# Kernel optimization log

Hardware: AMD Instinct MI355X
Metric: run time of the kernel (lower is better)

The kernel has to match this reference:

```python
import jax, jax.numpy as jnp
import numpy as np

B, AUDIO, FRAME = 4, 327680, 80
HID, NH, NKV, HD, FFN, NL = 320, 8, 4, 40, 1280, 6
WINDOWS = ((16, 4), (16, 4), (16, 0), (16, 0), (16, 4), (16, 4))


def _ln(x, w, eps=1e-5):
    m = x.mean(-1, keepdims=True)
    c = x - m
    v = (c * c).mean(-1, keepdims=True)
    return c * jax.lax.rsqrt(v + eps) * w


def _causal_conv(x, w, b, stride, left_pad):
    # x: [B, C_in, T]; w: [C_out, C_in, K] (torch Conv1d layout); causal left pad
    x = jnp.pad(x, ((0, 0), (0, 0), (left_pad, 0)))
    y = jax.lax.conv_general_dilated(x, w, (stride,), [(0, 0)],
                                     dimension_numbers=('NCH', 'OIH', 'NCH'))
    return y + b[None, :, None]


def _mask_conv(mask, stride, left_pad, ksize):
    # propagate bool validity mask through a strided causal conv
    mf = jnp.pad(mask.astype(jnp.float32)[:, None, :], ((0, 0), (0, 0), (left_pad, 0)))
    w1 = jnp.ones((1, 1, ksize), jnp.float32)
    mc = jax.lax.conv_general_dilated(mf, w1, (stride,), [(0, 0)],
                                      dimension_numbers=('NCH', 'OIH', 'NCH'))
    return mc[:, 0] > 0


def _window_mask(T, lw, rw, dtype):
    # additive mask: 0 where 0<=q-k<lw or 0<k-q<rw, else -inf; [1,1,T,T]
    d = jnp.arange(T)[:, None] - jnp.arange(T)[None, :]
    ok = ((d >= 0) & (d < lw)) | ((d < 0) & (-d < rw))
    return jnp.where(ok, jnp.zeros((), dtype), jnp.full((), -jnp.inf, dtype))[None, None]


def _encode(input_values, padding_mask, log_k, lin_w, conv1_w, conv1_b,
            conv2_w, conv2_b, ln1_w, q_w, k_w, v_w, o_w, ln2_w,
            fc1_w, fc2_w, final_ln_w):
    Bn = input_values.shape[0]
    x = input_values.reshape(Bn, -1, FRAME)               # [B, Tf, 80]
    # per-frame CMVN
    c = x - x.mean(-1, keepdims=True)
    x = c / jnp.sqrt((c * c).mean(-1, keepdims=True) + 1e-6)
    # learnable asinh compression
    x = jnp.arcsinh(jnp.exp(log_k) * x)
    x = jax.nn.silu(x @ lin_w.T)                          # [B, Tf, HID]
    Tf = x.shape[1]
    num_frames = padding_mask.sum(-1) // FRAME
    fmask = jnp.arange(Tf)[None, :] < num_frames[:, None]  # [B, Tf]
    x = x * fmask[..., None].astype(x.dtype)
    x = x.transpose(0, 2, 1)                              # [B, HID, Tf]
    # conv1: 320 -> 640, k=5, s=2, causal
    x = _causal_conv(x, conv1_w, conv1_b, 2, 4)
    m1 = _mask_conv(fmask, 2, 4, 5)
    x = jax.nn.silu(x * m1[:, None].astype(x.dtype))
    # conv2: 640 -> 320, k=5, s=2, causal
    m2 = _mask_conv(m1, 2, 4, 5)
    x = _causal_conv(x, conv2_w, conv2_b, 2, 4) * m2[:, None].astype(x.dtype)
    x = x.transpose(0, 2, 1)                              # [B, Tenc, HID]
    Tenc = x.shape[1]
    kpm = jnp.where(m2, jnp.zeros((), x.dtype), jnp.full((), -jnp.inf, x.dtype))[:, None, None, :]
    n_rep = NH // NKV
    scale = 1.0 / np.sqrt(HD).astype(np.float32)
    for i in range(NL):
        lw, rw = WINDOWS[i]
        wm = _window_mask(Tenc, lw, rw, x.dtype)
        h = _ln(x, ln1_w[i])
        q = (h @ q_w[i].T).reshape(Bn, Tenc, NH, HD).transpose(0, 2, 1, 3)
        k = (h @ k_w[i].T).reshape(Bn, Tenc, NKV, HD).transpose(0, 2, 1, 3)
        v = (h @ v_w[i].T).reshape(Bn, Tenc, NKV, HD).transpose(0, 2, 1, 3)
        k = jnp.repeat(k, n_rep, axis=1)                  # GQA repeat_kv
        v = jnp.repeat(v, n_rep, axis=1)
        s = jnp.einsum('bhqd,bhkd->bhqk', q, k) * scale + wm + kpm
        a = jax.nn.softmax(s, axis=-1)
        o = jnp.einsum('bhqk,bhkd->bhqd', a, v).transpose(0, 2, 1, 3).reshape(Bn, Tenc, HID)
        x = x + o @ o_w[i].T
        h = _ln(x, ln2_w[i])
        x = x + jax.nn.silu(h @ fc1_w[i].T) @ fc2_w[i].T
    return _ln(x, final_ln_w)


def setup_inputs() -> dict:
    key = jax.random.key(0)
    ks = iter(jax.random.split(key, 20))
    def w(shape, fan_in):
        return jax.random.normal(next(ks), shape, jnp.float32) / np.sqrt(fan_in).astype(np.float32)
    return {
        'input_values': jax.random.normal(next(ks), (B, AUDIO), jnp.float32),
        'padding_mask': jnp.ones((B, AUDIO), bool),
        'log_k': jnp.log(jnp.float32(0.75)),
        'lin_w': w((HID, FRAME), FRAME),
        'conv1_w': w((2 * HID, HID, 5), HID * 5), 'conv1_b': jnp.zeros((2 * HID,), jnp.float32),
        'conv2_w': w((HID, 2 * HID, 5), 2 * HID * 5), 'conv2_b': jnp.zeros((HID,), jnp.float32),
        'ln1_w': jnp.ones((NL, HID), jnp.float32),
        'q_w': w((NL, NH * HD, HID), HID),
        'k_w': w((NL, NKV * HD, HID), HID),
        'v_w': w((NL, NKV * HD, HID), HID),
        'o_w': w((NL, HID, NH * HD), NH * HD),
        'ln2_w': jnp.ones((NL, HID), jnp.float32),
        'fc1_w': w((NL, FFN, HID), HID),
        'fc2_w': w((NL, HID, FFN), FFN),
        'final_ln_w': jnp.ones((HID,), jnp.float32),
    }


def reference(input_values, padding_mask, log_k, lin_w, conv1_w, conv1_b,
              conv2_w, conv2_b, ln1_w, q_w, k_w, v_w, o_w, ln2_w,
              fc1_w, fc2_w, final_ln_w):
    return _encode(input_values, padding_mask, log_k, lin_w, conv1_w, conv1_b,
                   conv2_w, conv2_b, ln1_w, q_w, k_w, v_w, o_w, ln2_w,
                   fc1_w, fc2_w, final_ln_w)
```

## Files before the change

### kernel.cpp

```cpp
#include <hip/hip_runtime.h>
#include <hip/hip_bf16.h>
#include <math.h>


typedef __attribute__((ext_vector_type(8))) short short8;
typedef __attribute__((ext_vector_type(4))) float floatx4;

__device__ __forceinline__ float silu_f(float x) {
    return x / (1.0f + expf(-x));
}

__device__ __forceinline__ unsigned short f2bf(float x) {
    union { float f; unsigned int u; } v; v.f = x;
    unsigned int r = v.u + 0x7fffu + ((v.u >> 16) & 1u);
    return (unsigned short)(r >> 16);
}

__global__ void cvt_bf16(const float* __restrict__ s, unsigned short* __restrict__ d, int n) {
    int i = blockIdx.x * 256 + threadIdx.x;
    if (i < n) d[i] = f2bf(s[i]);
}

__global__ void pack_qkv(const float* __restrict__ qw, const float* __restrict__ kw,
                         const float* __restrict__ vw, unsigned short* __restrict__ d) {
    int i = blockIdx.x * 256 + threadIdx.x;
    if (i >= 6 * 640 * 320) return;
    int l = i / (640 * 320);
    int r = i - l * (640 * 320);
    int n = r / 320, c = r - (r / 320) * 320;
    float val;
    if (n < 320)      val = qw[((size_t)l * 320 + n) * 320 + c];
    else if (n < 480) val = kw[((size_t)l * 160 + (n - 320)) * 320 + c];
    else              val = vw[((size_t)l * 160 + (n - 480)) * 320 + c];
    d[i] = f2bf(val);
}

__global__ void prep_conv_w(const float* __restrict__ w, unsigned short* __restrict__ wt,
                            int Cout, int Cin) {
    int i = blockIdx.x * 256 + threadIdx.x;
    int total = Cout * Cin * 5;
    if (i >= total) return;
    int o = i / (Cin * 5);
    int rem = i - o * (Cin * 5);
    int c = rem / 5, k = rem - c * 5;
    wt[(size_t)o * (5 * Cin) + k * Cin + c] = f2bf(w[i]);
}

__global__ void prep_lin(const float* __restrict__ w, unsigned short* __restrict__ wt) {
    int i = blockIdx.x * 256 + threadIdx.x;
    if (i >= 320 * 128) return;
    int o = i >> 7, c = i & 127;
    wt[i] = (c < 80) ? f2bf(w[o * 80 + c]) : (unsigned short)0;
}

__global__ void cmvn_asinh_kernel(const float* __restrict__ in, const float* __restrict__ logk,
                                  unsigned short* __restrict__ zb) {
    __shared__ float raw[640];
    __shared__ float mS[8], iS[8];
    int f0 = blockIdx.x * 8;
    int tid = threadIdx.x;

    for (int e = tid; e < 640; e += 320)
        raw[e] = in[(size_t)f0 * 80 + e];
    __syncthreads();

    if (tid < 8) {
        float s = 0.f, ss = 0.f;
        for (int j = 0; j < 80; ++j) {
            float v = raw[tid * 80 + j];
            s += v; ss += v * v;
        }
        float m = s * (1.0f / 80.0f);
        float var = ss * (1.0f / 80.0f) - m * m;
        mS[tid] = m;
        iS[tid] = rsqrtf(var + 1e-6f);
    }
    __syncthreads();

    float ek = expf(logk[0]);
    for (int e = tid; e < 1024; e += 320) {
        int f = e >> 7, c = e & 127;
        unsigned short v = 0;
        if (c < 80) {
            float t = ek * (raw[f * 80 + c] - mS[f]) * iS[f];
            v = f2bf(asinhf(t));
        }
        zb[(size_t)(f0 + f) * 128 + c] = v;
    }
}

__global__ void im2col1(const unsigned short* __restrict__ x0, unsigned short* __restrict__ A1) {
    int idx = blockIdx.x * 256 + threadIdx.x;
    if (idx >= 8192 * 5 * 40) return;
    int c8 = idx % 40;
    int tmp = idx / 40;
    int kk = tmp % 5;
    int row = tmp / 5;
    int b = row >> 11, t = row & 2047;
    int sr = 2 * t + kk - 4;
    uint4 val = make_uint4(0u, 0u, 0u, 0u);
    if (sr >= 0) val = *(const uint4*)&x0[((size_t)b * 4096 + sr) * 320 + c8 * 8];
    *(uint4*)&A1[(size_t)row * 1600 + kk * 320 + c8 * 8] = val;
}

__global__ void im2col2(const unsigned short* __restrict__ y1, unsigned short* __restrict__ A2) {
    int idx = blockIdx.x * 256 + threadIdx.x;
    if (idx >= 4096 * 5 * 80) return;
    int c8 = idx % 80;
    int tmp = idx / 80;
    int kk = tmp % 5;
    int row = tmp / 5;
    int b = row >> 10, t = row & 1023;
    int sr = 2 * t + kk - 4;
    uint4 val = make_uint4(0u, 0u, 0u, 0u);
    if (sr >= 0) val = *(const uint4*)&y1[((size_t)b * 2048 + sr) * 640 + c8 * 8];
    *(uint4*)&A2[(size_t)row * 3200 + kk * 640 + c8 * 8] = val;
}

__global__ __launch_bounds__(256) void mfma_gemm(
    const unsigned short* __restrict__ A, const unsigned short* __restrict__ W,
    int M, int N, int K, int ldc,
    float* __restrict__ Cf, unsigned short* __restrict__ Cb,
    const float* __restrict__ bias, const float* __restrict__ res, int act_silu) {
    __shared__ unsigned short As[64 * 64];
    __shared__ unsigned short Bs[64 * 64];
    int m0 = blockIdx.x * 64;
    int n0 = blockIdx.y * 64;
    int tid = threadIdx.x;
    int wave = tid >> 6, lane = tid & 63;
    int lm = lane & 15, lq = lane >> 4;
    int wm = (wave & 1) * 32, wn = (wave >> 1) * 32;

    int lr = lane >> 3;
    int lg = (lane & 7) ^ lr;
    int rw0 = wave * 16;
    const unsigned short* a0 = A + (size_t)(m0 + rw0 + lr) * K + lg * 8;
    const unsigned short* a1 = A + (size_t)(m0 + rw0 + 8 + lr) * K + lg * 8;
    const unsigned short* b0 = W + (size_t)(n0 + rw0 + lr) * K + lg * 8;
    const unsigned short* b1 = W + (size_t)(n0 + rw0 + 8 + lr) * K + lg * 8;
    unsigned short* la0 = &As[rw0 * 64];
    unsigned short* la1 = &As[(rw0 + 8) * 64];
    unsigned short* lb0 = &Bs[rw0 * 64];
    unsigned short* lb1 = &Bs[(rw0 + 8) * 64];

    floatx4 acc[2][2];
#pragma unroll
    for (int i = 0; i < 2; ++i)
#pragma unroll
        for (int j = 0; j < 2; ++j) acc[i][j] = (floatx4)0.0f;

    int swl = lm & 7;

    for (int k0 = 0; k0 < K; k0 += 64) {
        __builtin_amdgcn_global_load_lds((const __attribute__((address_space(1))) void*)(a0 + k0),
                                         (__attribute__((address_space(3))) void*)la0, 16, 0, 0);
        __builtin_amdgcn_global_load_lds((const __attribute__((address_space(1))) void*)(a1 + k0),
                                         (__attribute__((address_space(3))) void*)la1, 16, 0, 0);
        __builtin_amdgcn_global_load_lds((const __attribute__((address_space(1))) void*)(b0 + k0),
                                         (__attribute__((address_space(3))) void*)lb0, 16, 0, 0);
        __builtin_amdgcn_global_load_lds((const __attribute__((address_space(1))) void*)(b1 + k0),
                                         (__attribute__((address_space(3))) void*)lb1, 16, 0, 0);
        __syncthreads();
#pragma unroll
        for (int ks = 0; ks < 2; ++ks) {
            int gg = ks * 4 + lq;
            short8 a[2], b[2];
#pragma unroll
            for (int i = 0; i < 2; ++i) {
                int r = wm + i * 16 + lm;
                a[i] = *(const short8*)&As[r * 64 + ((gg ^ swl)) * 8];
            }
#pragma unroll
            for (int j = 0; j < 2; ++j) {
                int r = wn + j * 16 + lm;
                b[j] = *(const short8*)&Bs[r * 64 + ((gg ^ swl)) * 8];
            }
#pragma unroll
            for (int i = 0; i < 2; ++i)
#pragma unroll
                for (int j = 0; j < 2; ++j)
                    acc[i][j] = __builtin_amdgcn_mfma_f32_16x16x32_bf16(a[i], b[j], acc[i][j], 0, 0, 0);
        }
        __syncthreads();
    }

#pragma unroll
    for (int j = 0; j < 2; ++j) {
        int n = n0 + wn + j * 16 + lm;
        float bv = bias ? bias[n] : 0.0f;
#pragma unroll
        for (int i = 0; i < 2; ++i) {
#pragma unroll
            for (int r = 0; r < 4; ++r) {
                int m = m0 + wm + i * 16 + lq * 4 + r;
                float v = acc[i][j][r] + bv;
                if (act_silu) v = silu_f(v);
                if (res) v += res[(size_t)m * ldc + n];
                if (Cf) Cf[(size_t)m * ldc + n] = v;
                else Cb[(size_t)m * ldc + n] = f2bf(v);
            }
        }
    }
}

__global__ __launch_bounds__(256) void ln_kernel(
    const float* __restrict__ x, const float* __restrict__ w,
    float* __restrict__ yf, unsigned short* __restrict__ yb) {
    int row = blockIdx.x * 4 + (threadIdx.x >> 6);
    int lane = threadIdx.x & 63;
    const float* xr = x + (size_t)row * 320;
    float v[5];
    float s = 0.f, ss = 0.f;
#pragma unroll
    for (int i = 0; i < 5; ++i) {
        v[i] = xr[lane + i * 64];
        s += v[i]; ss += v[i] * v[i];
    }
#pragma unroll
    for (int o = 32; o > 0; o >>= 1) {
        s += __shfl_down(s, o);
        ss += __shfl_down(ss, o);
    }
    s = __shfl(s, 0);
    ss = __shfl(ss, 0);
    float m = s * (1.0f / 320.0f);
    float rstd = rsqrtf(ss * (1.0f / 320.0f) - m * m + 1e-5f);
#pragma unroll
    for (int i = 0; i < 5; ++i) {
        float o_ = (v[i] - m) * rstd * w[lane + i * 64];
        if (yf) yf[(size_t)row * 320 + lane + i * 64] = o_;
        else yb[(size_t)row * 320 + lane + i * 64] = f2bf(o_);
    }
}

#define AROWS 82
#define APAD 44
__global__ __launch_bounds__(128) void attn_kernel(
    const float* __restrict__ qkv, unsigned short* __restrict__ o, int T, int rw) {
    __shared__ float Ks[AROWS * APAD];
    __shared__ float Vs[AROWS * APAD];
    int t0 = blockIdx.x * 64;
    int g = blockIdx.y, b = blockIdx.z;
    int tid = threadIdx.x;
    const float scale = 0.1581138830084190f;

    const float* base_k = qkv + (size_t)b * T * 640 + 320 + g * 40;
    const float* base_v = qkv + (size_t)b * T * 640 + 480 + g * 40;
    int rbase = t0 - 15;
    for (int idx = tid; idx < AROWS * 10; idx += 128) {
        int row = idx / 10, d4 = idx - row * 10;
        int gr = min(max(rbase + row, 0), T - 1);
        *(float4*)&Ks[row * APAD + d4 * 4] = *(const float4*)&base_k[(size_t)gr * 640 + d4 * 4];
        *(float4*)&Vs[row * APAD + d4 * 4] = *(const float4*)&base_v[(size_t)gr * 640 + d4 * 4];
    }
    __syncthreads();

    int q = tid >> 1;
    int hh = tid & 1;
    int t = t0 + q;
    int h = g * 2 + hh;

    const float* qrow = qkv + ((size_t)(b * T + t)) * 640 + h * 40;
    float qv[40];
#pragma unroll
    for (int d4 = 0; d4 < 10; ++d4) {
        float4 v4 = *(const float4*)&qrow[d4 * 4];
        qv[d4 * 4 + 0] = v4.x; qv[d4 * 4 + 1] = v4.y;
        qv[d4 * 4 + 2] = v4.z; qv[d4 * 4 + 3] = v4.w;
    }

    int kmaxoff = (rw > 0) ? (rw - 1) : 0;
    float s[19];
#pragma unroll
    for (int j = 0; j < 19; ++j) {
        int kk = t - 15 + j;
        const float* kr = &Ks[(q + j) * APAD];
        float acc = 0.f;
#pragma unroll
        for (int d4 = 0; d4 < 10; ++d4) {
            float4 k4 = *(const float4*)&kr[d4 * 4];
            acc = fmaf(qv[d4 * 4 + 0], k4.x, acc);
            acc = fmaf(qv[d4 * 4 + 1], k4.y, acc);
            acc = fmaf(qv[d4 * 4 + 2], k4.z, acc);
            acc = fmaf(qv[d4 * 4 + 3], k4.w, acc);
        }
        bool valid = (kk >= 0) && (kk < T) && (kk <= t + kmaxoff);
        s[j] = valid ? acc * scale : -1e30f;
    }

    float mx = -1e30f;
#pragma unroll
    for (int j = 0; j < 19; ++j) mx = fmaxf(mx, s[j]);
    float l = 0.f;
#pragma unroll
    for (int j = 0; j < 19; ++j) {
        s[j] = expf(s[j] - mx);
        l += s[j];
    }
    float inv = 1.0f / l;

    float ov[40];
#pragma unroll
    for (int d = 0; d < 40; ++d) ov[d] = 0.f;
#pragma unroll
    for (int j = 0; j < 19; ++j) {
        const float* vr = &Vs[(q + j) * APAD];
        float p = s[j] * inv;
#pragma unroll
        for (int d4 = 0; d4 < 10; ++d4) {
            float4 v4 = *(const float4*)&vr[d4 * 4];
            ov[d4 * 4 + 0] = fmaf(p, v4.x, ov[d4 * 4 + 0]);
            ov[d4 * 4 + 1] = fmaf(p, v4.y, ov[d4 * 4 + 1]);
            ov[d4 * 4 + 2] = fmaf(p, v4.z, ov[d4 * 4 + 2]);
            ov[d4 * 4 + 3] = fmaf(p, v4.w, ov[d4 * 4 + 3]);
        }
    }

    unsigned short* orow = o + ((size_t)(b * T + t)) * 320 + h * 40;
#pragma unroll
    for (int d2 = 0; d2 < 20; ++d2) {
        unsigned int lo = f2bf(ov[d2 * 2]);
        unsigned int hi = f2bf(ov[d2 * 2 + 1]);
        *(unsigned int*)&orow[d2 * 2] = lo | (hi << 16);
    }
}

extern "C" void kernel_launch(void* const* d_in, const int* in_sizes, int n_in,
                              void* d_out, int out_size, void* d_ws, size_t ws_size,
                              hipStream_t stream) {
    const float* input_values = (const float*)d_in[0];
    const float* log_k   = (const float*)d_in[2];
    const float* lin_w   = (const float*)d_in[3];
    const float* conv1_w = (const float*)d_in[4];
    const float* conv1_b = (const float*)d_in[5];
    const float* conv2_w = (const float*)d_in[6];
    const float* conv2_b = (const float*)d_in[7];
    const float* ln1_w   = (const float*)d_in[8];
    const float* q_w     = (const float*)d_in[9];
    const float* k_w     = (const float*)d_in[10];
    const float* v_w     = (const float*)d_in[11];
    const float* o_w     = (const float*)d_in[12];
    const float* ln2_w   = (const float*)d_in[13];
    const float* fc1_w   = (const float*)d_in[14];
    const float* fc2_w   = (const float*)d_in[15];
    const float* fln_w   = (const float*)d_in[16];
    float* out = (float*)d_out;

    unsigned char* wsb = (unsigned char*)d_ws;
    size_t off = 0;
    auto alloc = [&](size_t bytes) -> void* {
        void* p = wsb + off;
        off += (bytes + 255) & ~(size_t)255;
        return p;
    };

    unsigned short* im2 = (unsigned short*)alloc((size_t)8192 * 1600 * 2);
    unsigned short* x0  = (unsigned short*)alloc((size_t)16384 * 320 * 2);
    unsigned short* y1  = x0;
    unsigned short* f1  = im2;
    unsigned short* zb  = (unsigned short*)alloc((size_t)16384 * 128 * 2);
    float* xr   = (float*)alloc((size_t)4096 * 320 * 4);
    unsigned short* h = (unsigned short*)alloc((size_t)4096 * 320 * 2);
    float* qkvb = (float*)alloc((size_t)4096 * 640 * 4);
    unsigned short* ao = (unsigned short*)alloc((size_t)4096 * 320 * 2);
    unsigned short* wqkv = (unsigned short*)alloc((size_t)6 * 640 * 320 * 2);
    unsigned short* wo   = (unsigned short*)alloc((size_t)6 * 320 * 320 * 2);
    unsigned short* wf1  = (unsigned short*)alloc((size_t)6 * 1280 * 320 * 2);
    unsigned short* wf2  = (unsigned short*)alloc((size_t)6 * 320 * 1280 * 2);
    unsigned short* w1c  = (unsigned short*)alloc((size_t)640 * 1600 * 2);
    unsigned short* w2c  = (unsigned short*)alloc((size_t)320 * 3200 * 2);
    unsigned short* linb = (unsigned short*)alloc((size_t)320 * 128 * 2);

    prep_lin<<<dim3(160), 256, 0, stream>>>(lin_w, linb);
    pack_qkv<<<dim3((6 * 640 * 320 + 255) / 256), 256, 0, stream>>>(q_w, k_w, v_w, wqkv);
    cvt_bf16<<<dim3((614400 + 255) / 256), 256, 0, stream>>>(o_w, wo, 614400);
    cvt_bf16<<<dim3((2457600 + 255) / 256), 256, 0, stream>>>(fc1_w, wf1, 2457600);
    cvt_bf16<<<dim3((2457600 + 255) / 256), 256, 0, stream>>>(fc2_w, wf2, 2457600);
    prep_conv_w<<<dim3((640 * 320 * 5 + 255) / 256), 256, 0, stream>>>(conv1_w, w1c, 640, 320);
    prep_conv_w<<<dim3((320 * 640 * 5 + 255) / 256), 256, 0, stream>>>(conv2_w, w2c, 320, 640);

    cmvn_asinh_kernel<<<dim3(2048), 320, 0, stream>>>(input_values, log_k, zb);
    mfma_gemm<<<dim3(256, 5), 256, 0, stream>>>(zb, linb, 16384, 320, 128, 320,
                                                nullptr, x0, nullptr, nullptr, 1);

    im2col1<<<dim3((8192 * 5 * 40 + 255) / 256), 256, 0, stream>>>(x0, im2);
    mfma_gemm<<<dim3(128, 10), 256, 0, stream>>>(im2, w1c, 8192, 640, 1600, 640,
                                                 nullptr, y1, conv1_b, nullptr, 1);
    im2col2<<<dim3((4096 * 5 * 80 + 255) / 256), 256, 0, stream>>>(y1, im2);
    mfma_gemm<<<dim3(64, 5), 256, 0, stream>>>(im2, w2c, 4096, 320, 3200, 320,
                                               xr, nullptr, conv2_b, nullptr, 0);

    const int rws[6] = {4, 4, 0, 0, 4, 4};
    for (int l = 0; l < 6; ++l) {
        ln_kernel<<<1024, 256, 0, stream>>>(xr, ln1_w + l * 320, nullptr, h);
        mfma_gemm<<<dim3(64, 10), 256, 0, stream>>>(h, wqkv + (size_t)l * 204800,
                                                    4096, 640, 320, 640, qkvb, nullptr, nullptr, nullptr, 0);
        attn_kernel<<<dim3(16, 4, 4), 128, 0, stream>>>(qkvb, ao, 1024, rws[l]);
        mfma_gemm<<<dim3(64, 5), 256, 0, stream>>>(ao, wo + (size_t)l * 102400,
                                                   4096, 320, 320, 320, xr, nullptr, nullptr, xr, 0);
        ln_kernel<<<1024, 256, 0, stream>>>(xr, ln2_w + l * 320, nullptr, h);
        mfma_gemm<<<dim3(64, 20), 256, 0, stream>>>(h, wf1 + (size_t)l * 409600,
                                                    4096, 1280, 320, 1280, nullptr, f1, nullptr, nullptr, 1);
        mfma_gemm<<<dim3(64, 5), 256, 0, stream>>>(f1, wf2 + (size_t)l * 409600,
                                                   4096, 320, 1280, 320, xr, nullptr, nullptr, xr, 0);
    }
    ln_kernel<<<1024, 256, 0, stream>>>(xr, fln_w, out, nullptr);
}
```

Measured before the change: 662.0 us.

## Fuse im2col into implicit conv GEMM and merge weight prep kernels

Replaces the explicit im2col buffers and kernels for both strided causal convolutions with an implicit-GEMM conv kernel. It computes source row addresses per K-chunk and points padded rows at a small zero buffer. All seven weight conversion and packing launches are merged into one prep kernel. This removes a large im2col write and read round trip through global memory and several launch overheads. The trade-off is less contiguous A-tile loads, since rows are strided by two time steps.

```diff
diff --git a/kernel.cpp b/kernel.cpp
--- a/kernel.cpp
+++ b/kernel.cpp
@@ -16,41 +16,58 @@
     return (unsigned short)(r >> 16);
 }
 
-__global__ void cvt_bf16(const float* __restrict__ s, unsigned short* __restrict__ d, int n) {
-    int i = blockIdx.x * 256 + threadIdx.x;
-    if (i < n) d[i] = f2bf(s[i]);
-}
-
-__global__ void pack_qkv(const float* __restrict__ qw, const float* __restrict__ kw,
-                         const float* __restrict__ vw, unsigned short* __restrict__ d) {
-    int i = blockIdx.x * 256 + threadIdx.x;
-    if (i >= 6 * 640 * 320) return;
-    int l = i / (640 * 320);
-    int r = i - l * (640 * 320);
-    int n = r / 320, c = r - (r / 320) * 320;
-    float val;
-    if (n < 320)      val = qw[((size_t)l * 320 + n) * 320 + c];
-    else if (n < 480) val = kw[((size_t)l * 160 + (n - 320)) * 320 + c];
-    else              val = vw[((size_t)l * 160 + (n - 480)) * 320 + c];
-    d[i] = f2bf(val);
-}
-
-__global__ void prep_conv_w(const float* __restrict__ w, unsigned short* __restrict__ wt,
-                            int Cout, int Cin) {
-    int i = blockIdx.x * 256 + threadIdx.x;
-    int total = Cout * Cin * 5;
-    if (i >= total) return;
-    int o = i / (Cin * 5);
-    int rem = i - o * (Cin * 5);
-    int c = rem / 5, k = rem - c * 5;
-    wt[(size_t)o * (5 * Cin) + k * Cin + c] = f2bf(w[i]);
-}
-
-__global__ void prep_lin(const float* __restrict__ w, unsigned short* __restrict__ wt) {
-    int i = blockIdx.x * 256 + threadIdx.x;
-    if (i >= 320 * 128) return;
-    int o = i >> 7, c = i & 127;
-    wt[i] = (c < 80) ? f2bf(w[o * 80 + c]) : (unsigned short)0;
+__global__ void prep_all(
+    const float* __restrict__ lin_w, const float* __restrict__ qw,
+    const float* __restrict__ kw, const float* __restrict__ vw,
+    const float* __restrict__ ow, const float* __restrict__ f1w,
+    const float* __restrict__ f2w, const float* __restrict__ c1w,
+    const float* __restrict__ c2w,
+    unsigned short* __restrict__ linb, unsigned short* __restrict__ wqkv,
+    unsigned short* __restrict__ wo, unsigned short* __restrict__ wf1,
+    unsigned short* __restrict__ wf2, unsigned short* __restrict__ w1c,
+    unsigned short* __restrict__ w2c, unsigned short* __restrict__ zp) {
+    int idx = blockIdx.x * 256 + threadIdx.x;
+    if (idx < 40960) {
+        int o = idx >> 7, c = idx & 127;
+        linb[idx] = (c < 80) ? f2bf(lin_w[o * 80 + c]) : (unsigned short)0;
+        return;
+    }
+    idx -= 40960;
+    if (idx < 1228800) {
+        int l = idx / (640 * 320);
+        int r = idx - l * (640 * 320);
+        int n = r / 320, c = r - (r / 320) * 320;
+        float val;
+        if (n < 320)      val = qw[((size_t)l * 320 + n) * 320 + c];
+        else if (n < 480) val = kw[((size_t)l * 160 + (n - 320)) * 320 + c];
+        else              val = vw[((size_t)l * 160 + (n - 480)) * 320 + c];
+        wqkv[idx] = f2bf(val);
+        return;
+    }
+    idx -= 1228800;
+    if (idx < 614400) { wo[idx] = f2bf(ow[idx]); return; }
+    idx -= 614400;
+    if (idx < 2457600) { wf1[idx] = f2bf(f1w[idx]); return; }
+    idx -= 2457600;
+    if (idx < 2457600) { wf2[idx] = f2bf(f2w[idx]); return; }
+    idx -= 2457600;
+    if (idx < 1024000) {
+        int o = idx / 1600;
+        int rem = idx - o * 1600;
+        int k = rem / 320, c = rem - k * 320;
+        w1c[idx] = f2bf(c1w[(size_t)o * 1600 + c * 5 + k]);
+        return;
+    }
+    idx -= 1024000;
+    if (idx < 1024000) {
+        int o = idx / 3200;
+        int rem = idx - o * 3200;
+        int k = rem / 640, c = rem - k * 640;
+        w2c[idx] = f2bf(c2w[(size_t)o * 3200 + c * 5 + k]);
+        return;
+    }
+    idx -= 1024000;
+    if (idx < 64) zp[idx] = 0;
 }
 
 __global__ void cmvn_asinh_kernel(const float* __restrict__ in, const float* __restrict__ logk,
@@ -89,37 +106,9 @@
     }
 }
 
-__global__ void im2col1(const unsigned short* __restrict__ x0, unsigned short* __restrict__ A1) {
-    int idx = blockIdx.x * 256 + threadIdx.x;
-    if (idx >= 8192 * 5 * 40) return;
-    int c8 = idx % 40;
-    int tmp = idx / 40;
-    int kk = tmp % 5;
-    int row = tmp / 5;
-    int b = row >> 11, t = row & 2047;
-    int sr = 2 * t + kk - 4;
-    uint4 val = make_uint4(0u, 0u, 0u, 0u);
-    if (sr >= 0) val = *(const uint4*)&x0[((size_t)b * 4096 + sr) * 320 + c8 * 8];
-    *(uint4*)&A1[(size_t)row * 1600 + kk * 320 + c8 * 8] = val;
-}
-
-__global__ void im2col2(const unsigned short* __restrict__ y1, unsigned short* __restrict__ A2) {
-    int idx = blockIdx.x * 256 + threadIdx.x;
-    if (idx >= 4096 * 5 * 80) return;
-    int c8 = idx % 80;
-    int tmp = idx / 80;
-    int kk = tmp % 5;
-    int row = tmp / 5;
-    int b = row >> 10, t = row & 1023;
-    int sr = 2 * t + kk - 4;
-    uint4 val = make_uint4(0u, 0u, 0u, 0u);
-    if (sr >= 0) val = *(const uint4*)&y1[((size_t)b * 2048 + sr) * 640 + c8 * 8];
-    *(uint4*)&A2[(size_t)row * 3200 + kk * 640 + c8 * 8] = val;
-}
-
 __global__ __launch_bounds__(256) void mfma_gemm(
     const unsigned short* __restrict__ A, const unsigned short* __restrict__ W,
-    int M, int N, int K, int ldc,
+    int K, int ldc,
     float* __restrict__ Cf, unsigned short* __restrict__ Cb,
     const float* __restrict__ bias, const float* __restrict__ res, int act_silu) {
     __shared__ unsigned short As[64 * 64];
@@ -168,12 +157,12 @@
 #pragma unroll
             for (int i = 0; i < 2; ++i) {
                 int r = wm + i * 16 + lm;
-                a[i] = *(const short8*)&As[r * 64 + ((gg ^ swl)) * 8];
+                a[i] = *(const short8*)&As[r * 64 + (gg ^ swl) * 8];
             }
 #pragma unroll
             for (int j = 0; j < 2; ++j) {
                 int r = wn + j * 16 + lm;
-                b[j] = *(const short8*)&Bs[r * 64 + ((gg ^ swl)) * 8];
+                b[j] = *(const short8*)&Bs[r * 64 + (gg ^ swl) * 8];
             }
 #pragma unroll
             for (int i = 0; i < 2; ++i)
@@ -196,6 +185,105 @@
                 float v = acc[i][j][r] + bv;
                 if (act_silu) v = silu_f(v);
                 if (res) v += res[(size_t)m * ldc + n];
+                if (Cf) Cf[(size_t)m * ldc + n] = v;
+                else Cb[(size_t)m * ldc + n] = f2bf(v);
+            }
+        }
+    }
+}
+
+__global__ __launch_bounds__(256) void conv_gemm(
+    const unsigned short* __restrict__ X, const unsigned short* __restrict__ W,
+    const unsigned short* __restrict__ zp,
+    int Cin, int TinPerB, int ToutPerB, int ldc,
+    float* __restrict__ Cf, unsigned short* __restrict__ Cb,
+    const float* __restrict__ bias, int act_silu) {
+    __shared__ unsigned short As[64 * 64];
+    __shared__ unsigned short Bs[64 * 64];
+    int m0 = blockIdx.x * 64;
+    int n0 = blockIdx.y * 64;
+    int b = m0 / ToutPerB;
+    int t0 = m0 - b * ToutPerB;
+    int K5 = 5 * Cin;
+    int sub5 = Cin >> 6;
+    int nIter = 5 * sub5;
+    int tid = threadIdx.x;
+    int wave = tid >> 6, lane = tid & 63;
+    int lm = lane & 15, lq = lane >> 4;
+    int wm = (wave & 1) * 32, wn = (wave >> 1) * 32;
+
+    int lr = lane >> 3;
+    int lg = (lane & 7) ^ lr;
+    int rw0 = wave * 16;
+    const unsigned short* xb = X + (size_t)b * TinPerB * Cin;
+    int row0 = rw0 + lr, row1 = rw0 + 8 + lr;
+    const unsigned short* b0 = W + (size_t)(n0 + row0) * K5 + lg * 8;
+    const unsigned short* b1 = W + (size_t)(n0 + row1) * K5 + lg * 8;
+    unsigned short* la0 = &As[row0 * 64];
+    unsigned short* la1 = &As[row1 * 64];
+    unsigned short* lb0 = &Bs[row0 * 64];
+    unsigned short* lb1 = &Bs[row1 * 64];
+
+    floatx4 acc[2][2];
+#pragma unroll
+    for (int i = 0; i < 2; ++i)
+#pragma unroll
+        for (int j = 0; j < 2; ++j) acc[i][j] = (floatx4)0.0f;
+
+    int swl = lm & 7;
+
+    for (int it = 0; it < nIter; ++it) {
+        int kk = it / sub5;
+        int sub = it - kk * sub5;
+        int sr0 = 2 * (t0 + row0) + kk - 4;
+        int sr1 = 2 * (t0 + row1) + kk - 4;
+        const unsigned short* s0 = (sr0 >= 0)
+            ? xb + (size_t)sr0 * Cin + sub * 64 + lg * 8 : zp;
+        const unsigned short* s1 = (sr1 >= 0)
+            ? xb + (size_t)sr1 * Cin + sub * 64 + lg * 8 : zp;
+        __builtin_amdgcn_global_load_lds((const __attribute__((address_space(1))) void*)s0,
+                                         (__attribute__((address_space(3))) void*)la0, 16, 0, 0);
+        __builtin_amdgcn_global_load_lds((const __attribute__((address_space(1))) void*)s1,
+                                         (__attribute__((address_space(3))) void*)la1, 16, 0, 0);
+        __builtin_amdgcn_global_load_lds((const __attribute__((address_space(1))) void*)(b0 + it * 64),
+                                         (__attribute__((address_space(3))) void*)lb0, 16, 0, 0);
+        __builtin_amdgcn_global_load_lds((const __attribute__((address_space(1))) void*)(b1 + it * 64),
+                                         (__attribute__((address_space(3))) void*)lb1, 16, 0, 0);
+        __syncthreads();
+#pragma unroll
+        for (int ks = 0; ks < 2; ++ks) {
+            int gg = ks * 4 + lq;
+            short8 a[2], bb[2];
+#pragma unroll
+            for (int i = 0; i < 2; ++i) {
+                int r = wm + i * 16 + lm;
+                a[i] = *(const short8*)&As[r * 64 + (gg ^ swl) * 8];
+            }
+#pragma unroll
+            for (int j = 0; j < 2; ++j) {
+                int r = wn + j * 16 + lm;
+                bb[j] = *(const short8*)&Bs[r * 64 + (gg ^ swl) * 8];
+            }
+#pragma unroll
+            for (int i = 0; i < 2; ++i)
+#pragma unroll
+                for (int j = 0; j < 2; ++j)
+                    acc[i][j] = __builtin_amdgcn_mfma_f32_16x16x32_bf16(a[i], bb[j], acc[i][j], 0, 0, 0);
+        }
+        __syncthreads();
+    }
+
+#pragma unroll
+    for (int j = 0; j < 2; ++j) {
+        int n = n0 + wn + j * 16 + lm;
+        float bv = bias[n];
+#pragma unroll
+        for (int i = 0; i < 2; ++i) {
+#pragma unroll
+            for (int r = 0; r < 4; ++r) {
+                int m = m0 + wm + i * 16 + lq * 4 + r;
+                float v = acc[i][j][r] + bv;
+                if (act_silu) v = silu_f(v);
                 if (Cf) Cf[(size_t)m * ldc + n] = v;
                 else Cb[(size_t)m * ldc + n] = f2bf(v);
             }
@@ -354,55 +442,49 @@
         return p;
     };
 
-    unsigned short* im2 = (unsigned short*)alloc((size_t)8192 * 1600 * 2);
     unsigned short* x0  = (unsigned short*)alloc((size_t)16384 * 320 * 2);
-    unsigned short* y1  = x0;
-    unsigned short* f1  = im2;
+    unsigned short* y1  = (unsigned short*)alloc((size_t)8192 * 640 * 2);
+    unsigned short* f1  = (unsigned short*)alloc((size_t)4096 * 1280 * 2);
     unsigned short* zb  = (unsigned short*)alloc((size_t)16384 * 128 * 2);
     float* xr   = (float*)alloc((size_t)4096 * 320 * 4);
     unsigned short* h = (unsigned short*)alloc((size_t)4096 * 320 * 2);
     float* qkvb = (float*)alloc((size_t)4096 * 640 * 4);
     unsigned short* ao = (unsigned short*)alloc((size_t)4096 * 320 * 2);
+    unsigned short* linb = (unsigned short*)alloc((size_t)320 * 128 * 2);
     unsigned short* wqkv = (unsigned short*)alloc((size_t)6 * 640 * 320 * 2);
     unsigned short* wo   = (unsigned short*)alloc((size_t)6 * 320 * 320 * 2);
     unsigned short* wf1  = (unsigned short*)alloc((size_t)6 * 1280 * 320 * 2);
     unsigned short* wf2  = (unsigned short*)alloc((size_t)6 * 320 * 1280 * 2);
     unsigned short* w1c  = (unsigned short*)alloc((size_t)640 * 1600 * 2);
     unsigned short* w2c  = (unsigned short*)alloc((size_t)320 * 3200 * 2);
-    unsigned short* linb = (unsigned short*)alloc((size_t)320 * 128 * 2);
-
-    prep_lin<<<dim3(160), 256, 0, stream>>>(lin_w, linb);
-    pack_qkv<<<dim3((6 * 640 * 320 + 255) / 256), 256, 0, stream>>>(q_w, k_w, v_w, wqkv);
-    cvt_bf16<<<dim3((614400 + 255) / 256), 256, 0, stream>>>(o_w, wo, 614400);
-    cvt_bf16<<<dim3((2457600 + 255) / 256), 256, 0, stream>>>(fc1_w, wf1, 2457600);
-    cvt_bf16<<<dim3((2457600 + 255) / 256), 256, 0, stream>>>(fc2_w, wf2, 2457600);
-    prep_conv_w<<<dim3((640 * 320 * 5 + 255) / 256), 256, 0, stream>>>(conv1_w, w1c, 640, 320);
-    prep_conv_w<<<dim3((320 * 640 * 5 + 255) / 256), 256, 0, stream>>>(conv2_w, w2c, 320, 640);
+    unsigned short* zp   = (unsigned short*)alloc((size_t)64 * 2);
+
+    prep_all<<<dim3((8847424 + 255) / 256), 256, 0, stream>>>(
+        lin_w, q_w, k_w, v_w, o_w, fc1_w, fc2_w, conv1_w, conv2_w,
+        linb, wqkv, wo, wf1, wf2, w1c, w2c, zp);
 
     cmvn_asinh_kernel<<<dim3(2048), 320, 0, stream>>>(input_values, log_k, zb);
-    mfma_gemm<<<dim3(256, 5), 256, 0, stream>>>(zb, linb, 16384, 320, 128, 320,
+    mfma_gemm<<<dim3(256, 5), 256, 0, stream>>>(zb, linb, 128, 320,
                                                 nullptr, x0, nullptr, nullptr, 1);
 
-    im2col1<<<dim3((8192 * 5 * 40 + 255) / 256), 256, 0, stream>>>(x0, im2);
-    mfma_gemm<<<dim3(128, 10), 256, 0, stream>>>(im2, w1c, 8192, 640, 1600, 640,
-                                                 nullptr, y1, conv1_b, nullptr, 1);
-    im2col2<<<dim3((4096 * 5 * 80 + 255) / 256), 256, 0, stream>>>(y1, im2);
-    mfma_gemm<<<dim3(64, 5), 256, 0, stream>>>(im2, w2c, 4096, 320, 3200, 320,
-                                               xr, nullptr, conv2_b, nullptr, 0);
+    conv_gemm<<<dim3(128, 10), 256, 0, stream>>>(x0, w1c, zp, 320, 4096, 2048, 640,
+                                                 nullptr, y1, conv1_b, 1);
+    conv_gemm<<<dim3(64, 5), 256, 0, stream>>>(y1, w2c, zp, 640, 2048, 1024, 320,
+                                               xr, nullptr, conv2_b, 0);
 
     const int rws[6] = {4, 4, 0, 0, 4, 4};
     for (int l = 0; l < 6; ++l) {
         ln_kernel<<<1024, 256, 0, stream>>>(xr, ln1_w + l * 320, nullptr, h);
         mfma_gemm<<<dim3(64, 10), 256, 0, stream>>>(h, wqkv + (size_t)l * 204800,
-                                                    4096, 640, 320, 640, qkvb, nullptr, nullptr, nullptr, 0);
+                                                    320, 640, qkvb, nullptr, nullptr, nullptr, 0);
         attn_kernel<<<dim3(16, 4, 4), 128, 0, stream>>>(qkvb, ao, 1024, rws[l]);
         mfma_gemm<<<dim3(64, 5), 256, 0, stream>>>(ao, wo + (size_t)l * 102400,
-                                                   4096, 320, 320, 320, xr, nullptr, nullptr, xr, 0);
+                                                   320, 320, xr, nullptr, nullptr, xr, 0);
         ln_kernel<<<1024, 256, 0, stream>>>(xr, ln2_w + l * 320, nullptr, h);
         mfma_gemm<<<dim3(64, 20), 256, 0, stream>>>(h, wf1 + (size_t)l * 409600,
-                                                    4096, 1280, 320, 1280, nullptr, f1, nullptr, nullptr, 1);
+                                                    320, 1280, nullptr, f1, nullptr, nullptr, 1);
         mfma_gemm<<<dim3(64, 5), 256, 0, stream>>>(f1, wf2 + (size_t)l * 409600,
-                                                   4096, 320, 1280, 320, xr, nullptr, nullptr, xr, 0);
+                                                   1280, 320, xr, nullptr, nullptr, xr, 0);
     }
     ln_kernel<<<1024, 256, 0, stream>>>(xr, fln_w, out, nullptr);
 }
```

Result: faster. 620.6 us (-6.3%).
